# Optimization experiments

Measured on AMD Instinct MI355X. Metric: run time of the kernel, lower is better.

The kernel has to match this reference:

```python
import jax, jax.numpy as jnp
import numpy as np
from jax import lax

B, T, NL = 512, 1024, 64  # batch, seq_len, n_labels (tagset_size=62 -> +2 for start/stop)
NEG = -10000.0


def setup_inputs() -> dict:
    key = jax.random.key(0)
    k1, k2, k3 = jax.random.split(key, 3)
    logits = jax.random.normal(k1, (B, T, NL), dtype=jnp.float32)
    lens = jax.random.randint(k2, (B,), 0, T)
    transitions = jax.random.uniform(k3, (NL, NL), dtype=jnp.float32)  # uniform(0,1) as in init
    return {"logits": logits, "lens": lens, "transitions": transitions}


def reference(logits, lens, transitions):
    """CRF forward: log partition function. logits [B,T,L], lens [B], transitions [L,L]."""
    Bsz, Tlen, L = logits.shape
    start_idx, stop_idx = L - 2, L - 1
    alpha0 = jnp.full((Bsz, L), NEG, dtype=logits.dtype).at[:, start_idx].set(0.0)

    def step(carry, logit_t):
        alpha, c_lens = carry
        # mat[b,i,j] = trans[i,j] + alpha[b,j] + logit_t[b,i]
        mat = transitions[None, :, :] + alpha[:, None, :] + logit_t[:, :, None]
        alpha_nxt = jax.nn.logsumexp(mat, axis=2)  # [B,L]
        mask = (c_lens > 0)[:, None]
        alpha = jnp.where(mask, alpha_nxt, alpha)
        return (alpha, c_lens - 1), None

    (alpha, _), _ = lax.scan(step, (alpha0, lens), jnp.swapaxes(logits, 0, 1))
    alpha = alpha + transitions[stop_idx][None, :]
    return jax.nn.logsumexp(alpha, axis=1)  # [B]
```

## Files before the change

kernel.cpp:

```cpp
#include <hip/hip_runtime.h>

#define BATCH 512
#define TLEN  1024
#define NLAB  64
#define NEGV  -10000.0f

__global__ __launch_bounds__(64) void crf_fwd(
    const float* __restrict__ logits,
    const int*   __restrict__ lens,
    const float* __restrict__ trans,
    float*       __restrict__ out)
{
    const int lane = threadIdx.x;
    const int b = blockIdx.x;

    float Erow[NLAB];
    {
        const float4* tr4 = reinterpret_cast<const float4*>(trans + lane * NLAB);
        #pragma unroll
        for (int q = 0; q < NLAB / 4; ++q) {
            float4 v = tr4[q];
            Erow[4*q+0] = __expf(v.x); Erow[4*q+1] = __expf(v.y);
            Erow[4*q+2] = __expf(v.z); Erow[4*q+3] = __expf(v.w);
        }
    }

    const int len = lens[b];
    const float* lg = logits + (size_t)b * TLEN * NLAB + lane;
    auto ld = [&](int t) { int tc = t < TLEN ? t : TLEN - 1; return lg[tc * NLAB]; };

    const float tstart = trans[lane * NLAB + (NLAB - 2)];
    float a0 = (lane == NLAB - 2) ? 0.0f : NEGV;
    if (len > 0) a0 = ld(0) + tstart;
    float w = __expf(a0);
    float logS = 0.0f;

    float c[8], e[8];
    #pragma unroll
    for (int k = 0; k < 8; ++k) c[k] = ld(1 + k);
    #pragma unroll
    for (int k = 0; k < 8; ++k) e[k] = __expf(c[k]);

    for (int t0 = 1; t0 < len; t0 += 8) {
        float n[8];
        #pragma unroll
        for (int k = 0; k < 8; ++k) n[k] = ld(t0 + 8 + k);
        #pragma unroll
        for (int k = 0; k < 8; ++k) {
            if (t0 + k >= len) break;
            float el = e[k];
            if ((k & 3) == 0) {
                float s = __int_as_float(__builtin_amdgcn_readfirstlane(__float_as_int(w)));
                logS += __logf(s);
                el *= __builtin_amdgcn_rcpf(s);
            }
            const int wi = __float_as_int(w);
            float y0 = 0.f, y1 = 0.f, y2 = 0.f, y3 = 0.f;
            #pragma unroll
            for (int j = 0; j < NLAB; j += 4) {
                float w0 = __int_as_float(__builtin_amdgcn_readlane(wi, j + 0));
                float w1 = __int_as_float(__builtin_amdgcn_readlane(wi, j + 1));
                float w2 = __int_as_float(__builtin_amdgcn_readlane(wi, j + 2));
                float w3 = __int_as_float(__builtin_amdgcn_readlane(wi, j + 3));
                y0 = fmaf(w0, Erow[j + 0], y0);
                y1 = fmaf(w1, Erow[j + 1], y1);
                y2 = fmaf(w2, Erow[j + 2], y2);
                y3 = fmaf(w3, Erow[j + 3], y3);
            }
            w = ((y0 + y1) + (y2 + y3)) * el;
        }
        #pragma unroll
        for (int k = 0; k < 8; ++k) c[k] = n[k];
        #pragma unroll
        for (int k = 0; k < 8; ++k) e[k] = __expf(c[k]);
    }

    const float tstop = trans[(NLAB - 1) * NLAB + lane];
    float f = logS + __logf(w) + tstop;
    float m = f;
    #pragma unroll
    for (int o = 32; o > 0; o >>= 1) m = fmaxf(m, __shfl_xor(m, o));
    float s = __expf(f - m);
    #pragma unroll
    for (int o = 32; o > 0; o >>= 1) s += __shfl_xor(s, o);
    if (lane == 0) out[b] = m + __logf(s);
}

extern "C" void kernel_launch(void* const* d_in, const int* in_sizes, int n_in,
                              void* d_out, int out_size, void* d_ws, size_t ws_size,
                              hipStream_t stream) {
    const float* logits = (const float*)d_in[0];
    const int*   lens   = (const int*)d_in[1];
    const float* trans  = (const float*)d_in[2];
    float*       outp   = (float*)d_out;
    crf_fwd<<<BATCH, NLAB, 0, stream>>>(logits, lens, trans, outp);
}
```

Baseline: 389.2 us.

## Replace readlane broadcast matvec with DPP row-rotate and permlane swaps

The per-step 64x64 matvec no longer broadcasts each alpha value through 64 scalar readlanes. Each row-of-16 group instead uses permlane32/permlane16 swaps to obtain the four quarter-blocks of w, then 15 DPP row_ror fused multiply-accumulates per quarter. The transition exponentials are pre-permuted so each rotated operand lines up with the correct lane. This removes the SGPR round trip and readlane latency on the serial recurrence, at the cost of inline asm and DPP hazard-handling that depend on the gfx950 ISA.

```diff
diff --git a/kernel.cpp b/kernel.cpp
--- a/kernel.cpp
+++ b/kernel.cpp
@@ -4,6 +4,63 @@
 #define TLEN  1024
 #define NLAB  64
 #define NEGV  -10000.0f
+
+#define ROR_MOV(dst, src, K) \
+  asm("v_mov_b32_dpp %0, %1 row_ror:" #K " row_mask:0xf bank_mask:0xf" : "=v"(dst) : "v"(src))
+#define ROR_FMAC(acc, w, e, K) \
+  asm("v_fmac_f32_dpp %0, %1, %2 row_ror:" #K " row_mask:0xf bank_mask:0xf" : "+v"(acc) : "v"(w), "v"(e))
+
+__device__ __forceinline__ void swap32f(float &dst, float &src) {
+  asm("v_permlane32_swap_b32 %0, %1" : "+v"(dst), "+v"(src));
+}
+__device__ __forceinline__ void swap16f(float &dst, float &src) {
+  asm("v_permlane16_swap_b32 %0, %1" : "+v"(dst), "+v"(src));
+}
+__device__ __forceinline__ void swap32u(unsigned &dst, unsigned &src) {
+  asm("v_permlane32_swap_b32 %0, %1" : "+v"(dst), "+v"(src));
+}
+__device__ __forceinline__ void swap16u(unsigned &dst, unsigned &src) {
+  asm("v_permlane16_swap_b32 %0, %1" : "+v"(dst), "+v"(src));
+}
+
+#define SETUP_PHASE(Eq, S)                                  \
+  do {                                                      \
+    unsigned r_;                                            \
+    Eq[0] = __expf(tr[(S)]);                                \
+    ROR_MOV(r_, (S), 1);  Eq[1]  = __expf(tr[r_]);          \
+    ROR_MOV(r_, (S), 2);  Eq[2]  = __expf(tr[r_]);          \
+    ROR_MOV(r_, (S), 3);  Eq[3]  = __expf(tr[r_]);          \
+    ROR_MOV(r_, (S), 4);  Eq[4]  = __expf(tr[r_]);          \
+    ROR_MOV(r_, (S), 5);  Eq[5]  = __expf(tr[r_]);          \
+    ROR_MOV(r_, (S), 6);  Eq[6]  = __expf(tr[r_]);          \
+    ROR_MOV(r_, (S), 7);  Eq[7]  = __expf(tr[r_]);          \
+    ROR_MOV(r_, (S), 8);  Eq[8]  = __expf(tr[r_]);          \
+    ROR_MOV(r_, (S), 9);  Eq[9]  = __expf(tr[r_]);          \
+    ROR_MOV(r_, (S), 10); Eq[10] = __expf(tr[r_]);          \
+    ROR_MOV(r_, (S), 11); Eq[11] = __expf(tr[r_]);          \
+    ROR_MOV(r_, (S), 12); Eq[12] = __expf(tr[r_]);          \
+    ROR_MOV(r_, (S), 13); Eq[13] = __expf(tr[r_]);          \
+    ROR_MOV(r_, (S), 14); Eq[14] = __expf(tr[r_]);          \
+    ROR_MOV(r_, (S), 15); Eq[15] = __expf(tr[r_]);          \
+  } while (0)
+
+#define PHASE(T, Eq)                 \
+  y0 = fmaf((T), Eq[0], y0);         \
+  ROR_FMAC(y1, (T), Eq[1], 1);       \
+  ROR_FMAC(y2, (T), Eq[2], 2);       \
+  ROR_FMAC(y3, (T), Eq[3], 3);       \
+  ROR_FMAC(y0, (T), Eq[4], 4);       \
+  ROR_FMAC(y1, (T), Eq[5], 5);       \
+  ROR_FMAC(y2, (T), Eq[6], 6);       \
+  ROR_FMAC(y3, (T), Eq[7], 7);       \
+  ROR_FMAC(y0, (T), Eq[8], 8);       \
+  ROR_FMAC(y1, (T), Eq[9], 9);       \
+  ROR_FMAC(y2, (T), Eq[10], 10);     \
+  ROR_FMAC(y3, (T), Eq[11], 11);     \
+  ROR_FMAC(y0, (T), Eq[12], 12);     \
+  ROR_FMAC(y1, (T), Eq[13], 13);     \
+  ROR_FMAC(y2, (T), Eq[14], 14);     \
+  ROR_FMAC(y3, (T), Eq[15], 15);
 
 __global__ __launch_bounds__(64) void crf_fwd(
     const float* __restrict__ logits,
@@ -13,23 +70,37 @@
 {
     const int lane = threadIdx.x;
     const int b = blockIdx.x;
+    const float* tr = trans + lane * NLAB;
 
-    float Erow[NLAB];
-    {
-        const float4* tr4 = reinterpret_cast<const float4*>(trans + lane * NLAB);
-        #pragma unroll
-        for (int q = 0; q < NLAB / 4; ++q) {
-            float4 v = tr4[q];
-            Erow[4*q+0] = __expf(v.x); Erow[4*q+1] = __expf(v.y);
-            Erow[4*q+2] = __expf(v.z); Erow[4*q+3] = __expf(v.w);
-        }
-    }
+    unsigned pa = (unsigned)lane, pb, pc, pd;
+    pb = pa; swap32u(pb, pa);
+    pc = pa; swap16u(pc, pa);
+    pd = pb; swap16u(pd, pb);
+
+    float E0[16], E1[16], E2[16], E3[16];
+    SETUP_PHASE(E0, pc);
+    SETUP_PHASE(E1, pa);
+    SETUP_PHASE(E2, pd);
+    SETUP_PHASE(E3, pb);
 
     const int len = lens[b];
     const float* lg = logits + (size_t)b * TLEN * NLAB + lane;
     auto ld = [&](int t) { int tc = t < TLEN ? t : TLEN - 1; return lg[tc * NLAB]; };
 
-    const float tstart = trans[lane * NLAB + (NLAB - 2)];
+    auto matvec = [&](float wv) -> float {
+        float ta = wv, tb, tc, td;
+        tb = ta; swap32f(tb, ta);
+        tc = ta; swap16f(tc, ta);
+        td = tb; swap16f(td, tb);
+        float y0 = 0.f, y1 = 0.f, y2 = 0.f, y3 = 0.f;
+        PHASE(tc, E0)
+        PHASE(ta, E1)
+        PHASE(td, E2)
+        PHASE(tb, E3)
+        return (y0 + y1) + (y2 + y3);
+    };
+
+    const float tstart = tr[NLAB - 2];
     float a0 = (lane == NLAB - 2) ? 0.0f : NEGV;
     if (len > 0) a0 = ld(0) + tstart;
     float w = __expf(a0);
@@ -54,20 +125,7 @@
                 logS += __logf(s);
                 el *= __builtin_amdgcn_rcpf(s);
             }
-            const int wi = __float_as_int(w);
-            float y0 = 0.f, y1 = 0.f, y2 = 0.f, y3 = 0.f;
-            #pragma unroll
-            for (int j = 0; j < NLAB; j += 4) {
-                float w0 = __int_as_float(__builtin_amdgcn_readlane(wi, j + 0));
-                float w1 = __int_as_float(__builtin_amdgcn_readlane(wi, j + 1));
-                float w2 = __int_as_float(__builtin_amdgcn_readlane(wi, j + 2));
-                float w3 = __int_as_float(__builtin_amdgcn_readlane(wi, j + 3));
-                y0 = fmaf(w0, Erow[j + 0], y0);
-                y1 = fmaf(w1, Erow[j + 1], y1);
-                y2 = fmaf(w2, Erow[j + 2], y2);
-                y3 = fmaf(w3, Erow[j + 3], y3);
-            }
-            w = ((y0 + y1) + (y2 + y3)) * el;
+            w = matvec(w) * el;
         }
         #pragma unroll
         for (int k = 0; k < 8; ++k) c[k] = n[k];
```

Result: faster. 344.5 us (-11.5%).
